# Optimization experiments

Measured on AMD Instinct MI355X. Metric: run time of the kernel, lower is better.

## Reference

```python
import jax, jax.numpy as jnp
import numpy as np

L, D, H, FF = 6, 1024, 16, 4096
HD = D // H
EPS = 1e-5


def _ln(x, g, b):
    m = jnp.mean(x, axis=-1, keepdims=True)
    v = jnp.var(x, axis=-1, keepdims=True)
    return (x - m) * jax.lax.rsqrt(v + EPS) * g + b


def _heads(t, S, B):  # [S,B,D] -> [B*H,S,HD]
    return t.reshape(S, B * H, HD).swapaxes(0, 1)


def _attn(q, k, v, mask):
    # q,k,v: [B*H, Sq/Sk, HD]; q pre-scaled
    scores = jnp.einsum('bqd,bkd->bqk', q, k)
    if mask is not None:
        scores = scores + mask  # broadcast [1,Sq,Sk]
    p = jax.nn.softmax(scores, axis=-1)
    return jnp.einsum('bqk,bkd->bqd', p, v)


def _self_attn(x, w_qkv, b_qkv, w_out, b_out, mask):
    S, B, _ = x.shape
    qkv = x @ w_qkv.T + b_qkv  # [S,B,3D]
    q, k, v = jnp.split(qkv, 3, axis=-1)
    q = q * (HD ** -0.5)
    a = _attn(_heads(q, S, B), _heads(k, S, B), _heads(v, S, B), mask)
    a = a.swapaxes(0, 1).reshape(S, B, D)
    return a @ w_out.T + b_out


def _cross_attn(x, mem, w_q, b_q, w_kv, b_kv, w_out, b_out):
    S, B, _ = x.shape
    Sm = mem.shape[0]
    q = (x @ w_q.T + b_q) * (HD ** -0.5)
    kv = mem @ w_kv.T + b_kv  # [Sm,B,2D]
    k, v = jnp.split(kv, 2, axis=-1)
    a = _attn(_heads(q, S, B), _heads(k, Sm, B), _heads(v, Sm, B), None)
    a = a.swapaxes(0, 1).reshape(S, B, D)
    return a @ w_out.T + b_out


def _ffn(x, w1, b1, w2, b2):
    h = jax.nn.gelu(x @ w1.T + b1, approximate=False)
    return h @ w2.T + b2


def setup_inputs() -> dict:
    key = jax.random.key(0)
    ks = iter(jax.random.split(key, 64))
    def p(*shape, s=0.02):
        return (jax.random.normal(next(ks), shape, dtype=jnp.float32) * s)
    inp = {
        'src': jax.random.normal(next(ks), (512, 8, D), dtype=jnp.float32),
        'tgt': jax.random.normal(next(ks), (512, 8, D), dtype=jnp.float32),
        # encoder params (stacked over L layers)
        'enc_qkv_w': p(L, 3 * D, D), 'enc_qkv_b': p(L, 3 * D),
        'enc_out_w': p(L, D, D), 'enc_out_b': p(L, D),
        'enc_ln1_g': jnp.ones((L, D)), 'enc_ln1_b': jnp.zeros((L, D)),
        'enc_fc1_w': p(L, FF, D), 'enc_fc1_b': p(L, FF),
        'enc_fc2_w': p(L, D, FF), 'enc_fc2_b': p(L, D),
        'enc_ln2_g': jnp.ones((L, D)), 'enc_ln2_b': jnp.zeros((L, D)),
        'enc_norm_g': jnp.ones((D,)), 'enc_norm_b': jnp.zeros((D,)),
        # decoder params
        'dec_qkv_w': p(L, 3 * D, D), 'dec_qkv_b': p(L, 3 * D),
        'dec_sout_w': p(L, D, D), 'dec_sout_b': p(L, D),
        'dec_ln1_g': jnp.ones((L, D)), 'dec_ln1_b': jnp.zeros((L, D)),
        'dec_q_w': p(L, D, D), 'dec_q_b': p(L, D),
        'dec_kv_w': p(L, 2 * D, D), 'dec_kv_b': p(L, 2 * D),
        'dec_cout_w': p(L, D, D), 'dec_cout_b': p(L, D),
        'dec_ln2_g': jnp.ones((L, D)), 'dec_ln2_b': jnp.zeros((L, D)),
        'dec_fc1_w': p(L, FF, D), 'dec_fc1_b': p(L, FF),
        'dec_fc2_w': p(L, D, FF), 'dec_fc2_b': p(L, D),
        'dec_ln3_g': jnp.ones((L, D)), 'dec_ln3_b': jnp.zeros((L, D)),
        'dec_norm_g': jnp.ones((D,)), 'dec_norm_b': jnp.zeros((D,)),
    }
    return inp


def reference(src, tgt,
              enc_qkv_w, enc_qkv_b, enc_out_w, enc_out_b,
              enc_ln1_g, enc_ln1_b, enc_fc1_w, enc_fc1_b,
              enc_fc2_w, enc_fc2_b, enc_ln2_g, enc_ln2_b,
              enc_norm_g, enc_norm_b,
              dec_qkv_w, dec_qkv_b, dec_sout_w, dec_sout_b,
              dec_ln1_g, dec_ln1_b, dec_q_w, dec_q_b,
              dec_kv_w, dec_kv_b, dec_cout_w, dec_cout_b,
              dec_ln2_g, dec_ln2_b, dec_fc1_w, dec_fc1_b,
              dec_fc2_w, dec_fc2_b, dec_ln3_g, dec_ln3_b,
              dec_norm_g, dec_norm_b):
    St = tgt.shape[0]
    # causal additive mask [1,St,St]
    causal = jnp.where(jnp.tril(jnp.ones((St, St), dtype=bool)), 0.0, -jnp.inf)
    causal = causal[None].astype(src.dtype)

    # ---- encoder ----
    x = src
    for i in range(L):
        x = x + _self_attn(_ln(x, enc_ln1_g[i], enc_ln1_b[i]),
                           enc_qkv_w[i], enc_qkv_b[i], enc_out_w[i], enc_out_b[i], None)
        x = x + _ffn(_ln(x, enc_ln2_g[i], enc_ln2_b[i]),
                     enc_fc1_w[i], enc_fc1_b[i], enc_fc2_w[i], enc_fc2_b[i])
    memory = _ln(x, enc_norm_g, enc_norm_b)

    # ---- decoder ----
    y = tgt
    for i in range(L):
        y = y + _self_attn(_ln(y, dec_ln1_g[i], dec_ln1_b[i]),
                           dec_qkv_w[i], dec_qkv_b[i], dec_sout_w[i], dec_sout_b[i], causal)
        y = y + _cross_attn(_ln(y, dec_ln2_g[i], dec_ln2_b[i]), memory,
                            dec_q_w[i], dec_q_b[i], dec_kv_w[i], dec_kv_b[i],
                            dec_cout_w[i], dec_cout_b[i])
        y = y + _ffn(_ln(y, dec_ln3_g[i], dec_ln3_b[i]),
                     dec_fc1_w[i], dec_fc1_b[i], dec_fc2_w[i], dec_fc2_b[i])
    return _ln(y, dec_norm_g, dec_norm_b)
```

## Files before the change

### kernel.cpp

```cpp
#include <hip/hip_runtime.h>

typedef __attribute__((ext_vector_type(4))) float f32x4;
typedef __attribute__((ext_vector_type(8))) short short8;
typedef unsigned int u32;
typedef unsigned short u16;
typedef __attribute__((ext_vector_type(2))) u32 u32x2;
typedef __attribute__((ext_vector_type(4))) u32 u32x4;

#define DEV __device__ __forceinline__
#define SB0  __builtin_amdgcn_sched_barrier(0)
#define HBAR asm volatile("s_barrier" ::: "memory")

DEV u16 f2b(float f){
  u32 u = __builtin_bit_cast(u32, f);
  u32 r = u + 0x7fffu + ((u >> 16) & 1u);
  return (u16)(r >> 16);
}
DEV u32 pk2(float a, float b){ return (u32)f2b(a) | ((u32)f2b(b) << 16); }

DEV void gload16(const void* g, void* l){
  __builtin_amdgcn_global_load_lds((const __attribute__((address_space(1))) void*)g,
                                   (__attribute__((address_space(3))) void*)l, 16, 0, 0);
}
DEV u32 lds_addr(void* p){
  return (u32)(unsigned long long)(__attribute__((address_space(3))) char*)p;
}

__global__ __launch_bounds__(256) void cvt_k(const float* __restrict__ in,
                                             u16* __restrict__ out, int n8)
{
  int i = blockIdx.x*256 + threadIdx.x;
  const int stride = gridDim.x*256;
  for (; i < n8; i += stride){
    const float4 a = ((const float4*)in)[2*i];
    const float4 b = ((const float4*)in)[2*i+1];
    u32x4 r;
    r.x = pk2(a.x,a.y); r.y = pk2(a.z,a.w);
    r.z = pk2(b.x,b.y); r.w = pk2(b.z,b.w);
    ((u32x4*)out)[i] = r;
  }
}

template<int OUT_F32>
__global__ __launch_bounds__(256) void ln_k(const float* __restrict__ x,
    const float* __restrict__ gam, const float* __restrict__ bet,
    void* __restrict__ out)
{
  const int row = blockIdx.x, tid = threadIdx.x;
  const float4 v = ((const float4*)(x + row*1024))[tid];
  float s = (v.x + v.y) + (v.z + v.w);
  float q = (v.x*v.x + v.y*v.y) + (v.z*v.z + v.w*v.w);
  #pragma unroll
  for (int m = 1; m < 64; m <<= 1){ s += __shfl_xor(s, m); q += __shfl_xor(q, m); }
  __shared__ float ps[4], pq[4];
  if ((tid & 63) == 0){ ps[tid>>6] = s; pq[tid>>6] = q; }
  __syncthreads();
  s = (ps[0]+ps[1]) + (ps[2]+ps[3]);
  q = (pq[0]+pq[1]) + (pq[2]+pq[3]);
  const float mean = s * (1.f/1024.f);
  const float var  = q * (1.f/1024.f) - mean*mean;
  const float rstd = rsqrtf(var + 1e-5f);
  const float4 gg = ((const float4*)gam)[tid];
  const float4 bb = ((const float4*)bet)[tid];
  const float o0 = (v.x-mean)*rstd*gg.x + bb.x;
  const float o1 = (v.y-mean)*rstd*gg.y + bb.y;
  const float o2 = (v.z-mean)*rstd*gg.z + bb.z;
  const float o3 = (v.w-mean)*rstd*gg.w + bb.w;
  if (OUT_F32){
    float4 r; r.x=o0; r.y=o1; r.z=o2; r.w=o3;
    ((float4*)out)[row*256 + tid] = r;
  } else {
    u32x2 r; r.x = pk2(o0,o1); r.y = pk2(o2,o3);
    ((u32x2*)out)[row*256 + tid] = r;
  }
}

__global__ __launch_bounds__(256) void reduce4_k(const float* __restrict__ p,
    const float* __restrict__ res, const float* __restrict__ bias,
    float* __restrict__ out)
{
  const int row = blockIdx.x, tid = threadIdx.x;
  const size_t MN = 4096ull*1024ull;
  const float4 b  = ((const float4*)bias)[tid];
  const float4 a0 = ((const float4*)(p + 0*MN + (size_t)row*1024))[tid];
  const float4 a1 = ((const float4*)(p + 1*MN + (size_t)row*1024))[tid];
  const float4 a2 = ((const float4*)(p + 2*MN + (size_t)row*1024))[tid];
  const float4 a3 = ((const float4*)(p + 3*MN + (size_t)row*1024))[tid];
  const float4 r  = ((const float4*)(res + (size_t)row*1024))[tid];
  float4 o;
  o.x = (a0.x+a1.x)+(a2.x+a3.x) + r.x + b.x;
  o.y = (a0.y+a1.y)+(a2.y+a3.y) + r.y + b.y;
  o.z = (a0.z+a1.z)+(a2.z+a3.z) + r.z + b.z;
  o.w = (a0.w+a1.w)+(a2.w+a3.w) + r.w + b.w;
  ((float4*)(out + (size_t)row*1024))[tid] = o;
}

template<int DO_GELU>
__global__ __launch_bounds__(512,2) void gemm256_k(
    const u16* __restrict__ A, const u16* __restrict__ W,
    const float* __restrict__ bias, u16* __restrict__ Cout,
    int M, int N, int K)
{
  __shared__ char lds[131072];
  const int tid = threadIdx.x;
  const int lane = tid & 63, wid = tid >> 6;
  const int wr = wid >> 2, wc = wid & 3;
  const int g = lane >> 4, c16 = lane & 15;

  const u32 nwg = gridDim.x * gridDim.y;
  u32 flat = blockIdx.x + gridDim.x * blockIdx.y;
  {
    const u32 q = nwg >> 3, r = nwg & 7;
    const u32 xcd = flat & 7, idx = flat >> 3;
    flat = (xcd < r ? xcd*(q+1) : r*(q+1) + (xcd-r)*q) + idx;
  }
  const int m0 = (int)(flat % gridDim.x) * 256;
  const int n0 = (int)(flat / gridDim.x) * 256;

  f32x4 acc[8][4];
  #pragma unroll
  for (int m = 0; m < 8; m++)
    #pragma unroll
    for (int n = 0; n < 4; n++) acc[m][n] = (f32x4){0.f,0.f,0.f,0.f};

  const int srow = tid >> 3, schk = tid & 7;
  const int scg = schk ^ (srow & 7);
  const u16* aS = A + (size_t)(m0 + srow)*K + scg*8;
  const u16* wS = W + (size_t)(n0 + srow)*K + scg*8;

  auto SG = [&](const u16* base, int regionOff, int sb, int half, int i, int kk){
    gload16(base + (size_t)(half*128 + i*64)*K + kk,
            lds + sb*65536 + regionOff + half*16384 + i*8192 + tid*16);
  };
  short8 af[4][2], bf[4][2];
  auto LDA4 = [&](char* bufA, int mbase){
    #pragma unroll
    for (int i = 0; i < 4; i++){
      const int r = (mbase + i)*16 + c16;
      const int rx = r & 7;
      af[i][0] = *(const short8*)(bufA + r*128 + ((g ^ rx) << 4));
      af[i][1] = *(const short8*)(bufA + r*128 + (((4 + g) ^ rx) << 4));
    }
  };
  auto LDB2 = [&](char* bufB, int nbase){
    #pragma unroll
    for (int i = 0; i < 2; i++){
      const int r = (wc & 1)*64 + (nbase + i)*16 + c16;
      const int rx = r & 7;
      bf[nbase+i][0] = *(const short8*)(bufB + r*128 + ((g ^ rx) << 4));
      bf[nbase+i][1] = *(const short8*)(bufB + r*128 + (((4 + g) ^ rx) << 4));
    }
  };

  const int NT = K >> 6;
  SG(wS, 32768, 0, 0, 0, 0); SG(wS, 32768, 0, 0, 1, 0);
  SG(wS, 32768, 0, 1, 0, 0); SG(wS, 32768, 0, 1, 1, 0);
  SG(aS, 0,     0, 0, 0, 0); SG(aS, 0,     0, 0, 1, 0);
  SG(aS, 0,     0, 1, 0, 0); SG(aS, 0,     0, 1, 1, 0);
  asm volatile("s_waitcnt vmcnt(1)" ::: "memory");
  HBAR;

  for (int t = 0; t < NT; ++t){
    const int b = t & 1, sb = b ^ 1;
    const int skk = (t+1) << 6;
    const bool st = (t+1 < NT);
    char* bufA = lds + b*65536 + wr*16384;
    char* bufB = lds + b*65536 + 32768 + (wc >> 1)*16384;

    LDA4(bufA, 0); LDB2(bufB, 0);
    if (st){ SG(wS, 32768, sb, 0, 0, skk); SG(wS, 32768, sb, 0, 1, skk); }
    HBAR;
    asm volatile("s_waitcnt lgkmcnt(0)" ::: "memory"); SB0;
    __builtin_amdgcn_s_setprio(1);
    #pragma unroll
    for (int ks = 0; ks < 2; ks++)
      #pragma unroll
      for (int i = 0; i < 4; i++)
        #pragma unroll
        for (int j = 0; j < 2; j++)
          acc[i][j] = __builtin_amdgcn_mfma_f32_16x16x32_bf16(af[i][ks], bf[j][ks], acc[i][j], 0,0,0);
    __builtin_amdgcn_s_setprio(0);
    LDB2(bufB, 2);
    if (st){ SG(wS, 32768, sb, 1, 0, skk); SG(wS, 32768, sb, 1, 1, skk); }
    HBAR;
    asm volatile("s_waitcnt lgkmcnt(0)" ::: "memory"); SB0;
    __builtin_amdgcn_s_setprio(1);
    #pragma unroll
    for (int ks = 0; ks < 2; ks++)
      #pragma unroll
      for (int i = 0; i < 4; i++)
        #pragma unroll
        for (int j = 2; j < 4; j++)
          acc[i][j] = __builtin_amdgcn_mfma_f32_16x16x32_bf16(af[i][ks], bf[j][ks], acc[i][j], 0,0,0);
    __builtin_amdgcn_s_setprio(0);
    if (st) asm volatile("s_waitcnt vmcnt(4)" ::: "memory");
    else    asm volatile("s_waitcnt vmcnt(0)" ::: "memory");
    HBAR;
    LDA4(bufA, 4);
    if (st){ SG(aS, 0, sb, 0, 0, skk); SG(aS, 0, sb, 0, 1, skk); }
    asm volatile("s_waitcnt lgkmcnt(0)" ::: "memory"); SB0;
    __builtin_amdgcn_s_setprio(1);
    #pragma unroll
    for (int ks = 0; ks < 2; ks++)
      #pragma unroll
      for (int i = 0; i < 4; i++)
        #pragma unroll
        for (int j = 0; j < 2; j++)
          acc[4+i][j] = __builtin_amdgcn_mfma_f32_16x16x32_bf16(af[i][ks], bf[j][ks], acc[4+i][j], 0,0,0);
    __builtin_amdgcn_s_setprio(0);
    if (st){ SG(aS, 0, sb, 1, 0, skk); SG(aS, 0, sb, 1, 1, skk); }
    HBAR;
    __builtin_amdgcn_s_setprio(1);
    #pragma unroll
    for (int ks = 0; ks < 2; ks++)
      #pragma unroll
      for (int i = 0; i < 4; i++)
        #pragma unroll
        for (int j = 2; j < 4; j++)
          acc[4+i][j] = __builtin_amdgcn_mfma_f32_16x16x32_bf16(af[i][ks], bf[j][ks], acc[4+i][j], 0,0,0);
    __builtin_amdgcn_s_setprio(0);
    if (st) asm volatile("s_waitcnt vmcnt(1)" ::: "memory");
    HBAR;
  }

  #pragma unroll
  for (int n = 0; n < 4; n++){
    const int col = n0 + wc*64 + n*16 + c16;
    const float bv = bias[col];
    #pragma unroll
    for (int m = 0; m < 8; m++){
      const int rbase = m0 + wr*128 + m*16 + g*4;
      #pragma unroll
      for (int r = 0; r < 4; r++){
        float v = acc[m][n][r] + bv;
        if (DO_GELU) v = 0.5f*v*(1.f + erff(v*0.70710678118654752f));
        Cout[(size_t)(rbase + r)*N + col] = f2b(v);
      }
    }
  }
}

template<int DO_GELU, int DO_RES, int OUT_F32>
__global__ __launch_bounds__(512,2) void gemm128p_k(
    const u16* __restrict__ A, const u16* __restrict__ W,
    const float* __restrict__ bias, const float* __restrict__ res,
    void* __restrict__ Cout, int M, int N, int K)
{
  __shared__ char lds[65536];
  const int tid = threadIdx.x;
  const int lane = tid & 63, wid = tid >> 6;
  const int wr = wid >> 2, wc = wid & 3;
  const int g = lane >> 4, c16 = lane & 15;

  const u32 nwg = gridDim.x * gridDim.y;
  u32 flat = blockIdx.x + gridDim.x * blockIdx.y;
  {
    const u32 q = nwg >> 3, r = nwg & 7;
    const u32 xcd = flat & 7, idx = flat >> 3;
    flat = (xcd < r ? xcd*(q+1) : r*(q+1) + (xcd-r)*q) + idx;
  }
  const int n0 = (int)(flat % gridDim.x) * 128;
  const int m0 = (int)(flat / gridDim.x) * 128;

  f32x4 acc[4][2];
  #pragma unroll
  for (int m = 0; m < 4; m++)
    #pragma unroll
    for (int n = 0; n < 2; n++) acc[m][n] = (f32x4){0.f,0.f,0.f,0.f};

  const int srow = tid >> 3, schk = tid & 7;
  const int scg = schk ^ (srow & 7);
  const u16* aS = A + (size_t)(m0 + srow)*K + scg*8;
  const u16* wS = W + (size_t)(n0 + srow)*K + scg*8;

  auto SG = [&](const u16* base, int regionOff, int sb, int i, int kk){
    gload16(base + (size_t)(i*64)*K + kk,
            lds + sb*32768 + regionOff + i*8192 + tid*16);
  };
  short8 af[2][2], af2[2][2], bf[2][2];
  auto LDA = [&](short8 (*dst)[2], char* bufA, int mbase){
    #pragma unroll
    for (int i = 0; i < 2; i++){
      const int r = wr*64 + (mbase + i)*16 + c16;
      const int rx = r & 7;
      dst[i][0] = *(const short8*)(bufA + r*128 + ((g ^ rx) << 4));
      dst[i][1] = *(const short8*)(bufA + r*128 + (((4 + g) ^ rx) << 4));
    }
  };
  auto LDB = [&](char* bufB){
    #pragma unroll
    for (int i = 0; i < 2; i++){
      const int r = wc*32 + i*16 + c16;
      const int rx = r & 7;
      bf[i][0] = *(const short8*)(bufB + r*128 + ((g ^ rx) << 4));
      bf[i][1] = *(const short8*)(bufB + r*128 + (((4 + g) ^ rx) << 4));
    }
  };

  const int NT = K >> 6;
  SG(wS, 16384, 0, 0, 0); SG(wS, 16384, 0, 1, 0);
  SG(aS, 0,     0, 0, 0); SG(aS, 0,     0, 1, 0);

  for (int t = 0; t < NT; ++t){
    const int b = t & 1, sb = b ^ 1;
    const int skk = (t+1) << 6;
    const bool st = (t+1 < NT);
    char* bufA = lds + b*32768;
    char* bufB = lds + b*32768 + 16384;

    if (st){ SG(wS, 16384, sb, 0, skk); SG(wS, 16384, sb, 1, skk); }
    if (st) asm volatile("s_waitcnt vmcnt(2)" ::: "memory");
    else    asm volatile("s_waitcnt vmcnt(0)" ::: "memory");
    HBAR;
    LDA(af, bufA, 0); LDB(bufB);
    if (st){ SG(aS, 0, sb, 0, skk); SG(aS, 0, sb, 1, skk); }
    asm volatile("s_waitcnt lgkmcnt(0)" ::: "memory"); SB0;
    __builtin_amdgcn_s_setprio(1);
    #pragma unroll
    for (int ks = 0; ks < 2; ks++)
      #pragma unroll
      for (int i = 0; i < 2; i++)
        #pragma unroll
        for (int j = 0; j < 2; j++)
          acc[i][j] = __builtin_amdgcn_mfma_f32_16x16x32_bf16(af[i][ks], bf[j][ks], acc[i][j], 0,0,0);
    __builtin_amdgcn_s_setprio(0);
    LDA(af2, bufA, 2);
    asm volatile("s_waitcnt lgkmcnt(0)" ::: "memory"); SB0;
    __builtin_amdgcn_s_setprio(1);
    #pragma unroll
    for (int ks = 0; ks < 2; ks++)
      #pragma unroll
      for (int i = 0; i < 2; i++)
        #pragma unroll
        for (int j = 0; j < 2; j++)
          acc[2+i][j] = __builtin_amdgcn_mfma_f32_16x16x32_bf16(af2[i][ks], bf[j][ks], acc[2+i][j], 0,0,0);
    __builtin_amdgcn_s_setprio(0);
    HBAR;
  }

  #pragma unroll
  for (int n = 0; n < 2; n++){
    const int col = n0 + wc*32 + n*16 + c16;
    const float bv = bias[col];
    #pragma unroll
    for (int m = 0; m < 4; m++){
      const int rbase = m0 + wr*64 + m*16 + g*4;
      #pragma unroll
      for (int r = 0; r < 4; r++){
        float v = acc[m][n][r] + bv;
        if (DO_GELU) v = 0.5f*v*(1.f + erff(v*0.70710678118654752f));
        if (DO_RES)  v += res[(size_t)(rbase + r)*N + col];
        if (OUT_F32) ((float*)Cout)[(size_t)(rbase + r)*N + col] = v;
        else         ((u16*)Cout)[(size_t)(rbase + r)*N + col] = f2b(v);
      }
    }
  }
}

__global__ __launch_bounds__(512,2) void gemmsk_k(
    const u16* __restrict__ A, const u16* __restrict__ W,
    float* __restrict__ part, int M, int N, int Kfull)
{
  __shared__ char lds[65536];
  const int tid = threadIdx.x;
  const int lane = tid & 63, wid = tid >> 6;
  const int wr = wid >> 2, wc = wid & 3;
  const int g = lane >> 4, c16 = lane & 15;
  const int k0 = (int)blockIdx.z << 10;

  const u32 nwg = gridDim.x * gridDim.y;
  u32 flat = blockIdx.x + gridDim.x * blockIdx.y;
  {
    const u32 q = nwg >> 3, r = nwg & 7;
    const u32 xcd = flat & 7, idx = flat >> 3;
    flat = (xcd < r ? xcd*(q+1) : r*(q+1) + (xcd-r)*q) + idx;
  }
  const int n0 = (int)(flat % gridDim.x) * 128;
  const int m0 = (int)(flat / gridDim.x) * 128;

  f32x4 acc[4][2];
  #pragma unroll
  for (int m = 0; m < 4; m++)
    #pragma unroll
    for (int n = 0; n < 2; n++) acc[m][n] = (f32x4){0.f,0.f,0.f,0.f};

  const int srow = tid >> 3, schk = tid & 7;
  const int scg = schk ^ (srow & 7);
  const u16* aS = A + (size_t)(m0 + srow)*Kfull + k0 + scg*8;
  const u16* wS = W + (size_t)(n0 + srow)*Kfull + k0 + scg*8;

  auto SG = [&](const u16* base, int regionOff, int sb, int i, int kk){
    gload16(base + (size_t)(i*64)*Kfull + kk,
            lds + sb*32768 + regionOff + i*8192 + tid*16);
  };
  short8 af[2][2], af2[2][2], bf[2][2];
  auto LDA = [&](short8 (*dst)[2], char* bufA, int mbase){
    #pragma unroll
    for (int i = 0; i < 2; i++){
      const int r = wr*64 + (mbase + i)*16 + c16;
      const int rx = r & 7;
      dst[i][0] = *(const short8*)(bufA + r*128 + ((g ^ rx) << 4));
      dst[i][1] = *(const short8*)(bufA + r*128 + (((4 + g) ^ rx) << 4));
    }
  };
  auto LDB = [&](char* bufB){
    #pragma unroll
    for (int i = 0; i < 2; i++){
      const int r = wc*32 + i*16 + c16;
      const int rx = r & 7;
      bf[i][0] = *(const short8*)(bufB + r*128 + ((g ^ rx) << 4));
      bf[i][1] = *(const short8*)(bufB + r*128 + (((4 + g) ^ rx) << 4));
    }
  };

  const int NT = 16;
  SG(wS, 16384, 0, 0, 0); SG(wS, 16384, 0, 1, 0);
  SG(aS, 0,     0, 0, 0); SG(aS, 0,     0, 1, 0);

  for (int t = 0; t < NT; ++t){
    const int b = t & 1, sb = b ^ 1;
    const int skk = (t+1) << 6;
    const bool st = (t+1 < NT);
    char* bufA = lds + b*32768;
    char* bufB = lds + b*32768 + 16384;

    if (st){ SG(wS, 16384, sb, 0, skk); SG(wS, 16384, sb, 1, skk); }
    if (st) asm volatile("s_waitcnt vmcnt(2)" ::: "memory");
    else    asm volatile("s_waitcnt vmcnt(0)" ::: "memory");
    HBAR;
    LDA(af, bufA, 0); LDB(bufB);
    if (st){ SG(aS, 0, sb, 0, skk); SG(aS, 0, sb, 1, skk); }
    asm volatile("s_waitcnt lgkmcnt(0)" ::: "memory"); SB0;
    __builtin_amdgcn_s_setprio(1);
    #pragma unroll
    for (int ks = 0; ks < 2; ks++)
      #pragma unroll
      for (int i = 0; i < 2; i++)
        #pragma unroll
        for (int j = 0; j < 2; j++)
          acc[i][j] = __builtin_amdgcn_mfma_f32_16x16x32_bf16(af[i][ks], bf[j][ks], acc[i][j], 0,0,0);
    __builtin_amdgcn_s_setprio(0);
    LDA(af2, bufA, 2);
    asm volatile("s_waitcnt lgkmcnt(0)" ::: "memory"); SB0;
    __builtin_amdgcn_s_setprio(1);
    #pragma unroll
    for (int ks = 0; ks < 2; ks++)
      #pragma unroll
      for (int i = 0; i < 2; i++)
        #pragma unroll
        for (int j = 0; j < 2; j++)
          acc[2+i][j] = __builtin_amdgcn_mfma_f32_16x16x32_bf16(af2[i][ks], bf[j][ks], acc[2+i][j], 0,0,0);
    __builtin_amdgcn_s_setprio(0);
    HBAR;
  }

  float* out = part + (size_t)blockIdx.z * ((size_t)M * N);
  #pragma unroll
  for (int n = 0; n < 2; n++){
    const int col = n0 + wc*32 + n*16 + c16;
    #pragma unroll
    for (int m = 0; m < 4; m++){
      const int rbase = m0 + wr*64 + m*16 + g*4;
      #pragma unroll
      for (int r = 0; r < 4; r++)
        out[(size_t)(rbase + r)*N + col] = acc[m][n][r];
    }
  }
}

template<int CAUSAL>
__global__ __launch_bounds__(256,4) void attn_k(
    const u16* __restrict__ Qb, int qB, int qS,
    const u16* __restrict__ Kb, int kB, int kS,
    const u16* __restrict__ Vb, int vB, int vS,
    u16* __restrict__ Ob, int oB, int oS, float scale)
{
  __shared__ char smem[32768];
  const int tid = threadIdx.x;
  const int lane = tid & 63, w = tid >> 6;
  const int g = lane >> 4, c16 = lane & 15;
  const int qt = blockIdx.x, bh = blockIdx.y;
  const int b = bh >> 4, h = bh & 15;
  const u16* Q  = Qb + b*qB + h*64;
  const u16* Kp = Kb + b*kB + h*64;
  const u16* Vp = Vb + b*vB + h*64;
  u16*       Op = Ob + b*oB + h*64;

  const int qrow = qt*64 + w*16 + c16;
  const short8 bq0 = *(const short8*)(Q + qrow*qS + g*8);
  const short8 bq1 = *(const short8*)(Q + qrow*qS + 32 + g*8);

  f32x4 o[4];
  #pragma unroll
  for (int d = 0; d < 4; d++) o[d] = (f32x4){0.f,0.f,0.f,0.f};
  float mrun = -__builtin_inff(), lrun = 0.f;

  const int srow = tid >> 3, schk = tid & 7;
  const u16* kSrc = Kp + srow*kS + (schk ^ (srow & 7))*8;
  const u16* vSrc = Vp + srow*vS + schk*8;
  const u32 vtr0 = lds_addr(smem) + 16384 + (8*g + (c16 >> 2))*128 + (c16 & 3)*8;

  auto STAGE = [&](int p, int j0){
    char* kb = smem + p*8192 + w*1024;
    char* vb = smem + 16384 + p*8192 + w*1024;
    gload16(kSrc + (size_t)j0*kS, kb);
    gload16(kSrc + (size_t)(j0+32)*kS, kb + 4096);
    gload16(vSrc + (size_t)j0*vS, vb);
    gload16(vSrc + (size_t)(j0+32)*vS, vb + 4096);
  };
  auto COMPUTE = [&](int p, int j0){
    char* Ks = smem + p*8192;
    f32x4 st[4];
    #pragma unroll
    for (int t = 0; t < 4; t++){
      const int row = t*16 + c16;
      const int rx = row & 7;
      const short8 ka0 = *(const short8*)(Ks + row*128 + ((g ^ rx) << 4));
      const short8 ka1 = *(const short8*)(Ks + row*128 + (((4 + g) ^ rx) << 4));
      f32x4 z = (f32x4){0.f,0.f,0.f,0.f};
      z = __builtin_amdgcn_mfma_f32_16x16x32_bf16(ka0, bq0, z, 0,0,0);
      z = __builtin_amdgcn_mfma_f32_16x16x32_bf16(ka1, bq1, z, 0,0,0);
      st[t] = z;
    }
    float mloc = -__builtin_inff();
    #pragma unroll
    for (int t = 0; t < 4; t++)
      #pragma unroll
      for (int r = 0; r < 4; r++){
        float sv = st[t][r]*scale;
        if (CAUSAL){ if (j0 + t*16 + g*4 + r > qrow) sv = -__builtin_inff(); }
        st[t][r] = sv;
        mloc = fmaxf(mloc, sv);
      }
    mloc = fmaxf(mloc, __shfl_xor(mloc, 16));
    mloc = fmaxf(mloc, __shfl_xor(mloc, 32));
    const float mnew = fmaxf(mrun, mloc);
    const float corr = __expf(mrun - mnew);
    float psum = 0.f;
    u32 pk[4][2];
    #pragma unroll
    for (int t = 0; t < 4; t++){
      const float p0 = __expf(st[t][0]-mnew), p1 = __expf(st[t][1]-mnew);
      const float p2 = __expf(st[t][2]-mnew), p3 = __expf(st[t][3]-mnew);
      psum += (p0+p1) + (p2+p3);
      pk[t][0] = pk2(p0,p1); pk[t][1] = pk2(p2,p3);
    }
    psum += __shfl_xor(psum, 16);
    psum += __shfl_xor(psum, 32);
    lrun = lrun*corr + psum;
    mrun = mnew;
    #pragma unroll
    for (int d = 0; d < 4; d++){
      o[d][0]*=corr; o[d][1]*=corr; o[d][2]*=corr; o[d][3]*=corr;
    }
    const int sl0 = c16 | (((g << 1)     & 3) << 4);
    const int sl1 = c16 | ((((g << 1)+1) & 3) << 4);
    const bool hi = g >= 2;
    union { short8 s; u32 u[4]; } pb, pb2;
    {
      const u32 a00 = (u32)__shfl((int)pk[0][0], sl0), a01 = (u32)__shfl((int)pk[0][1], sl0);
      const u32 a02 = (u32)__shfl((int)pk[0][0], sl1), a03 = (u32)__shfl((int)pk[0][1], sl1);
      const u32 a10 = (u32)__shfl((int)pk[1][0], sl0), a11 = (u32)__shfl((int)pk[1][1], sl0);
      const u32 a12 = (u32)__shfl((int)pk[1][0], sl1), a13 = (u32)__shfl((int)pk[1][1], sl1);
      pb.u[0] = hi ? a10 : a00;
      pb.u[1] = hi ? a11 : a01;
      pb.u[2] = hi ? a12 : a02;
      pb.u[3] = hi ? a13 : a03;
    }
    {
      const u32 a00 = (u32)__shfl((int)pk[2][0], sl0), a01 = (u32)__shfl((int)pk[2][1], sl0);
      const u32 a02 = (u32)__shfl((int)pk[2][0], sl1), a03 = (u32)__shfl((int)pk[2][1], sl1);
      const u32 a10 = (u32)__shfl((int)pk[3][0], sl0), a11 = (u32)__shfl((int)pk[3][1], sl0);
      const u32 a12 = (u32)__shfl((int)pk[3][0], sl1), a13 = (u32)__shfl((int)pk[3][1], sl1);
      pb2.u[0] = hi ? a10 : a00;
      pb2.u[1] = hi ? a11 : a01;
      pb2.u[2] = hi ? a12 : a02;
      pb2.u[3] = hi ? a13 : a03;
    }

    const u32 vtr = vtr0 + p*8192;
    u32x2 t00,t01,t10,t11,t20,t21,t30,t31;
    asm volatile("ds_read_b64_tr_b16 %0, %1 offset:0"   : "=v"(t00) : "v"(vtr));
    asm volatile("ds_read_b64_tr_b16 %0, %1 offset:512" : "=v"(t01) : "v"(vtr));
    asm volatile("ds_read_b64_tr_b16 %0, %1 offset:32"  : "=v"(t10) : "v"(vtr));
    asm volatile("ds_read_b64_tr_b16 %0, %1 offset:544" : "=v"(t11) : "v"(vtr));
    asm volatile("ds_read_b64_tr_b16 %0, %1 offset:64"  : "=v"(t20) : "v"(vtr));
    asm volatile("ds_read_b64_tr_b16 %0, %1 offset:576" : "=v"(t21) : "v"(vtr));
    asm volatile("ds_read_b64_tr_b16 %0, %1 offset:96"  : "=v"(t30) : "v"(vtr));
    asm volatile("ds_read_b64_tr_b16 %0, %1 offset:608" : "=v"(t31) : "v"(vtr));
    asm volatile("s_waitcnt lgkmcnt(0)" ::: "memory");
    __builtin_amdgcn_sched_barrier(0);
    {
      union { short8 s; u32x2 d[2]; } v0u, v1u, v2u, v3u;
      v0u.d[0]=t00; v0u.d[1]=t01;
      v1u.d[0]=t10; v1u.d[1]=t11;
      v2u.d[0]=t20; v2u.d[1]=t21;
      v3u.d[0]=t30; v3u.d[1]=t31;
      o[0] = __builtin_amdgcn_mfma_f32_16x16x32_bf16(v0u.s, pb.s, o[0], 0,0,0);
      o[1] = __builtin_amdgcn_mfma_f32_16x16x32_bf16(v1u.s, pb.s, o[1], 0,0,0);
      o[2] = __builtin_amdgcn_mfma_f32_16x16x32_bf16(v2u.s, pb.s, o[2], 0,0,0);
      o[3] = __builtin_amdgcn_mfma_f32_16x16x32_bf16(v3u.s, pb.s, o[3], 0,0,0);
    }
    asm volatile("ds_read_b64_tr_b16 %0, %1 offset:4096" : "=v"(t00) : "v"(vtr));
    asm volatile("ds_read_b64_tr_b16 %0, %1 offset:4608" : "=v"(t01) : "v"(vtr));
    asm volatile("ds_read_b64_tr_b16 %0, %1 offset:4128" : "=v"(t10) : "v"(vtr));
    asm volatile("ds_read_b64_tr_b16 %0, %1 offset:4640" : "=v"(t11) : "v"(vtr));
    asm volatile("ds_read_b64_tr_b16 %0, %1 offset:4160" : "=v"(t20) : "v"(vtr));
    asm volatile("ds_read_b64_tr_b16 %0, %1 offset:4672" : "=v"(t21) : "v"(vtr));
    asm volatile("ds_read_b64_tr_b16 %0, %1 offset:4192" : "=v"(t30) : "v"(vtr));
    asm volatile("ds_read_b64_tr_b16 %0, %1 offset:4704" : "=v"(t31) : "v"(vtr));
    asm volatile("s_waitcnt lgkmcnt(0)" ::: "memory");
    __builtin_amdgcn_sched_barrier(0);
    {
      union { short8 s; u32x2 d[2]; } v0u, v1u, v2u, v3u;
      v0u.d[0]=t00; v0u.d[1]=t01;
      v1u.d[0]=t10; v1u.d[1]=t11;
      v2u.d[0]=t20; v2u.d[1]=t21;
      v3u.d[0]=t30; v3u.d[1]=t31;
      o[0] = __builtin_amdgcn_mfma_f32_16x16x32_bf16(v0u.s, pb2.s, o[0], 0,0,0);
      o[1] = __builtin_amdgcn_mfma_f32_16x16x32_bf16(v1u.s, pb2.s, o[1], 0,0,0);
      o[2] = __builtin_amdgcn_mfma_f32_16x16x32_bf16(v2u.s, pb2.s, o[2], 0,0,0);
      o[3] = __builtin_amdgcn_mfma_f32_16x16x32_bf16(v3u.s, pb2.s, o[3], 0,0,0);
    }
  };

  const int nCh = CAUSAL ? (qt + 1) : 8;
  STAGE(0, 0);
  for (int jc = 0; jc < nCh - 1; ++jc){
    STAGE((jc+1) & 1, (jc+1)*64);
    asm volatile("s_waitcnt vmcnt(4)" ::: "memory");
    HBAR; SB0;
    COMPUTE(jc & 1, jc*64);
    SB0; HBAR;
  }
  asm volatile("s_waitcnt vmcnt(0)" ::: "memory");
  HBAR; SB0;
  COMPUTE((nCh-1) & 1, (nCh-1)*64);
  SB0; HBAR;

  const float inv = 1.f / lrun;
  char* Olds = smem;
  #pragma unroll
  for (int dd = 0; dd < 4; dd++){
    u32x2 val;
    val.x = pk2(o[dd][0]*inv, o[dd][1]*inv);
    val.y = pk2(o[dd][2]*inv, o[dd][3]*inv);
    const int row = w*16 + c16;
    const int off = 32*dd + 8*g;
    const int chunk = off >> 4, rem = off & 15;
    *(u32x2*)(Olds + row*128 + ((chunk ^ (row & 7)) << 4) + rem) = val;
  }
  __syncthreads();
  const int orow = tid >> 2, oc = tid & 3;
  #pragma unroll
  for (int i = 0; i < 2; i++){
    const int ch = oc*2 + i;
    const u32x4 vv = *(const u32x4*)(Olds + orow*128 + ((ch ^ (orow & 7)) << 4));
    *(u32x4*)(Op + (qt*64 + orow)*oS + ch*8) = vv;
  }
}

static inline int cvt_grid(int n8){ int g = (n8 + 255) / 256; return g > 2048 ? 2048 : g; }

extern "C" void kernel_launch(void* const* d_in, const int* in_sizes, int n_in,
                              void* d_out, int out_size, void* d_ws, size_t ws_size,
                              hipStream_t stream)
{
  (void)in_sizes; (void)n_in; (void)out_size; (void)ws_size;
  const float* src      = (const float*)d_in[0];
  const float* tgt      = (const float*)d_in[1];
  const float* e_qkv_w  = (const float*)d_in[2];
  const float* e_qkv_b  = (const float*)d_in[3];
  const float* e_out_w  = (const float*)d_in[4];
  const float* e_out_b  = (const float*)d_in[5];
  const float* e_ln1_g  = (const float*)d_in[6];
  const float* e_ln1_b  = (const float*)d_in[7];
  const float* e_fc1_w  = (const float*)d_in[8];
  const float* e_fc1_b  = (const float*)d_in[9];
  const float* e_fc2_w  = (const float*)d_in[10];
  const float* e_fc2_b  = (const float*)d_in[11];
  const float* e_ln2_g  = (const float*)d_in[12];
  const float* e_ln2_b  = (const float*)d_in[13];
  const float* e_nrm_g  = (const float*)d_in[14];
  const float* e_nrm_b  = (const float*)d_in[15];
  const float* dc_qkv_w = (const float*)d_in[16];
  const float* dc_qkv_b = (const float*)d_in[17];
  const float* dc_sout_w= (const float*)d_in[18];
  const float* dc_sout_b= (const float*)d_in[19];
  const float* dc_ln1_g = (const float*)d_in[20];
  const float* dc_ln1_b = (const float*)d_in[21];
  const float* dc_q_w   = (const float*)d_in[22];
  const float* dc_q_b   = (const float*)d_in[23];
  const float* dc_kv_w  = (const float*)d_in[24];
  const float* dc_kv_b  = (const float*)d_in[25];
  const float* dc_cout_w= (const float*)d_in[26];
  const float* dc_cout_b= (const float*)d_in[27];
  const float* dc_ln2_g = (const float*)d_in[28];
  const float* dc_ln2_b = (const float*)d_in[29];
  const float* dc_fc1_w = (const float*)d_in[30];
  const float* dc_fc1_b = (const float*)d_in[31];
  const float* dc_fc2_w = (const float*)d_in[32];
  const float* dc_fc2_b = (const float*)d_in[33];
  const float* dc_ln3_g = (const float*)d_in[34];
  const float* dc_ln3_b = (const float*)d_in[35];
  const float* dc_nrm_g = (const float*)d_in[36];
  const float* dc_nrm_b = (const float*)d_in[37];

  char* ws = (char*)d_ws;
  u16*  ln_out = (u16*)(ws);
  u16*  attn_o = (u16*)(ws + (8u<<20));
  u16*  membuf = (u16*)(ws + (16u<<20));
  float* xres  = (float*)(ws + (24u<<20));
  u16*  region = (u16*)(ws + (40u<<20));
  u16*  qkv   = region;
  u16*  hbuf  = region;
  u16*  qbuf  = region;
  u16*  kvbuf = region + (4u<<20);
  float* fparts = (float*)(ws + (432ull<<20));

  const dim3 blk(256);
  const dim3 blk512(512);
  const int M = 4096;

  u16* wb = (u16*)(ws + (72u<<20));
  size_t woff = 0;
  auto CV = [&](const float* wsrc, size_t n)->u16* {
    u16* p = wb + woff; woff += n;
    cvt_k<<<cvt_grid((int)(n >> 3)), blk, 0, stream>>>(wsrc, p, (int)(n >> 3));
    return p;
  };
  u16* Weqkv = CV(e_qkv_w,  6ull*3072*1024);
  u16* Weout = CV(e_out_w,  6ull*1024*1024);
  u16* Wefc1 = CV(e_fc1_w,  6ull*4096*1024);
  u16* Wefc2 = CV(e_fc2_w,  6ull*4096*1024);
  u16* Wdqkv = CV(dc_qkv_w, 6ull*3072*1024);
  u16* Wdsout= CV(dc_sout_w,6ull*1024*1024);
  u16* Wdq   = CV(dc_q_w,   6ull*1024*1024);
  u16* Wdkv  = CV(dc_kv_w,  6ull*2048*1024);
  u16* Wdcout= CV(dc_cout_w,6ull*1024*1024);
  u16* Wdfc1 = CV(dc_fc1_w, 6ull*4096*1024);
  u16* Wdfc2 = CV(dc_fc2_w, 6ull*4096*1024);

  for (int i = 0; i < 6; i++){
    const float* xin = i ? xres : src;
    ln_k<0><<<4096, blk, 0, stream>>>(xin, e_ln1_g + i*1024, e_ln1_b + i*1024, ln_out);
    gemm256_k<0><<<dim3(16, 12), blk512, 0, stream>>>(ln_out,
        Weqkv + (size_t)i*3145728, e_qkv_b + i*3072, qkv, M, 3072, 1024);
    attn_k<0><<<dim3(8,128), blk, 0, stream>>>(qkv, 3072, 24576,
        qkv+1024, 3072, 24576, qkv+2048, 3072, 24576, attn_o, 1024, 8192, 0.125f);
    gemm128p_k<0,1,1><<<dim3(8, 32), blk512, 0, stream>>>(attn_o,
        Weout + (size_t)i*1048576, e_out_b + i*1024, xin, xres, M, 1024, 1024);
    ln_k<0><<<4096, blk, 0, stream>>>(xres, e_ln2_g + i*1024, e_ln2_b + i*1024, ln_out);
    gemm256_k<1><<<dim3(16, 16), blk512, 0, stream>>>(ln_out,
        Wefc1 + (size_t)i*4194304, e_fc1_b + i*4096, hbuf, M, 4096, 1024);
    gemmsk_k<<<dim3(8, 32, 4), blk512, 0, stream>>>(hbuf,
        Wefc2 + (size_t)i*4194304, fparts, M, 1024, 4096);
    reduce4_k<<<4096, blk, 0, stream>>>(fparts, xres, e_fc2_b + i*1024, xres);
  }
  ln_k<0><<<4096, blk, 0, stream>>>(xres, e_nrm_g, e_nrm_b, membuf);

  for (int i = 0; i < 6; i++){
    const float* yin = i ? xres : tgt;
    ln_k<0><<<4096, blk, 0, stream>>>(yin, dc_ln1_g + i*1024, dc_ln1_b + i*1024, ln_out);
    gemm256_k<0><<<dim3(16, 12), blk512, 0, stream>>>(ln_out,
        Wdqkv + (size_t)i*3145728, dc_qkv_b + i*3072, qkv, M, 3072, 1024);
    attn_k<1><<<dim3(8,128), blk, 0, stream>>>(qkv, 3072, 24576,
        qkv+1024, 3072, 24576, qkv+2048, 3072, 24576, attn_o, 1024, 8192, 0.125f);
    gemm128p_k<0,1,1><<<dim3(8, 32), blk512, 0, stream>>>(attn_o,
        Wdsout + (size_t)i*1048576, dc_sout_b + i*1024, yin, xres, M, 1024, 1024);
    ln_k<0><<<4096, blk, 0, stream>>>(xres, dc_ln2_g + i*1024, dc_ln2_b + i*1024, ln_out);
    gemm128p_k<0,0,0><<<dim3(8, 32), blk512, 0, stream>>>(ln_out,
        Wdq + (size_t)i*1048576, dc_q_b + i*1024, nullptr, qbuf, M, 1024, 1024);
    gemm128p_k<0,0,0><<<dim3(16, 32), blk512, 0, stream>>>(membuf,
        Wdkv + (size_t)i*2097152, dc_kv_b + i*2048, nullptr, kvbuf, M, 2048, 1024);
    attn_k<0><<<dim3(8,128), blk, 0, stream>>>(qbuf, 1024, 8192,
        kvbuf, 2048, 16384, kvbuf+1024, 2048, 16384, attn_o, 1024, 8192, 0.125f);
    gemm128p_k<0,1,1><<<dim3(8, 32), blk512, 0, stream>>>(attn_o,
        Wdcout + (size_t)i*1048576, dc_cout_b + i*1024, xres, xres, M, 1024, 1024);
    ln_k<0><<<4096, blk, 0, stream>>>(xres, dc_ln3_g + i*1024, dc_ln3_b + i*1024, ln_out);
    gemm256_k<1><<<dim3(16, 16), blk512, 0, stream>>>(ln_out,
        Wdfc1 + (size_t)i*4194304, dc_fc1_b + i*4096, hbuf, M, 4096, 1024);
    gemmsk_k<<<dim3(8, 32, 4), blk512, 0, stream>>>(hbuf,
        Wdfc2 + (size_t)i*4194304, fparts, M, 1024, 4096);
    reduce4_k<<<4096, blk, 0, stream>>>(fparts, xres, dc_fc2_b + i*1024, xres);
  }
  ln_k<1><<<4096, blk, 0, stream>>>(xres, dc_nrm_g, dc_nrm_b, d_out);
}
```

Before: 3.362 ms.

## Replace split-K FC2 with fused full-K GEMM and merge cross-attn projections

FC2 no longer uses the 4-way split-K GEMM with fp32 partials and a separate reduce kernel. It now calls the 128-tile GEMM over the full K with bias and residual fused into the epilogue. The decoder's cross-attention Q and KV projections are combined into one launch through a new dual-GEMM kernel that splits workgroups between the two problems. This removes the partial-sum memory traffic and extra launches, at the cost of fewer workgroups and longer serial K loops for FC2.

```diff
diff --git a/kernel.cpp b/kernel.cpp
--- a/kernel.cpp
+++ b/kernel.cpp
@@ -75,26 +75,6 @@
   }
 }
 
-__global__ __launch_bounds__(256) void reduce4_k(const float* __restrict__ p,
-    const float* __restrict__ res, const float* __restrict__ bias,
-    float* __restrict__ out)
-{
-  const int row = blockIdx.x, tid = threadIdx.x;
-  const size_t MN = 4096ull*1024ull;
-  const float4 b  = ((const float4*)bias)[tid];
-  const float4 a0 = ((const float4*)(p + 0*MN + (size_t)row*1024))[tid];
-  const float4 a1 = ((const float4*)(p + 1*MN + (size_t)row*1024))[tid];
-  const float4 a2 = ((const float4*)(p + 2*MN + (size_t)row*1024))[tid];
-  const float4 a3 = ((const float4*)(p + 3*MN + (size_t)row*1024))[tid];
-  const float4 r  = ((const float4*)(res + (size_t)row*1024))[tid];
-  float4 o;
-  o.x = (a0.x+a1.x)+(a2.x+a3.x) + r.x + b.x;
-  o.y = (a0.y+a1.y)+(a2.y+a3.y) + r.y + b.y;
-  o.z = (a0.z+a1.z)+(a2.z+a3.z) + r.z + b.z;
-  o.w = (a0.w+a1.w)+(a2.w+a3.w) + r.w + b.w;
-  ((float4*)(out + (size_t)row*1024))[tid] = o;
-}
-
 template<int DO_GELU>
 __global__ __launch_bounds__(512,2) void gemm256_k(
     const u16* __restrict__ A, const u16* __restrict__ W,
@@ -240,6 +220,105 @@
   }
 }
 
+DEV void g128_body(const u16* __restrict__ A, const u16* __restrict__ W,
+                   const float* __restrict__ bias, u16* __restrict__ Cout,
+                   int N, int K, int m0, int n0, char* lds)
+{
+  const int tid = threadIdx.x;
+  const int lane = tid & 63, wid = tid >> 6;
+  const int wr = wid >> 2, wc = wid & 3;
+  const int g = lane >> 4, c16 = lane & 15;
+
+  f32x4 acc[4][2];
+  #pragma unroll
+  for (int m = 0; m < 4; m++)
+    #pragma unroll
+    for (int n = 0; n < 2; n++) acc[m][n] = (f32x4){0.f,0.f,0.f,0.f};
+
+  const int srow = tid >> 3, schk = tid & 7;
+  const int scg = schk ^ (srow & 7);
+  const u16* aS = A + (size_t)(m0 + srow)*K + scg*8;
+  const u16* wS = W + (size_t)(n0 + srow)*K + scg*8;
+
+  auto SG = [&](const u16* base, int regionOff, int sb, int i, int kk){
+    gload16(base + (size_t)(i*64)*K + kk,
+            lds + sb*32768 + regionOff + i*8192 + tid*16);
+  };
+  short8 af[2][2], af2[2][2], bf[2][2];
+  auto LDA = [&](short8 (*dst)[2], char* bufA, int mbase){
+    #pragma unroll
+    for (int i = 0; i < 2; i++){
+      const int r = wr*64 + (mbase + i)*16 + c16;
+      const int rx = r & 7;
+      dst[i][0] = *(const short8*)(bufA + r*128 + ((g ^ rx) << 4));
+      dst[i][1] = *(const short8*)(bufA + r*128 + (((4 + g) ^ rx) << 4));
+    }
+  };
+  auto LDB = [&](char* bufB){
+    #pragma unroll
+    for (int i = 0; i < 2; i++){
+      const int r = wc*32 + i*16 + c16;
+      const int rx = r & 7;
+      bf[i][0] = *(const short8*)(bufB + r*128 + ((g ^ rx) << 4));
+      bf[i][1] = *(const short8*)(bufB + r*128 + (((4 + g) ^ rx) << 4));
+    }
+  };
+
+  const int NT = K >> 6;
+  SG(wS, 16384, 0, 0, 0); SG(wS, 16384, 0, 1, 0);
+  SG(aS, 0,     0, 0, 0); SG(aS, 0,     0, 1, 0);
+
+  for (int t = 0; t < NT; ++t){
+    const int b = t & 1, sb = b ^ 1;
+    const int skk = (t+1) << 6;
+    const bool st = (t+1 < NT);
+    char* bufA = lds + b*32768;
+    char* bufB = lds + b*32768 + 16384;
+
+    if (st){ SG(wS, 16384, sb, 0, skk); SG(wS, 16384, sb, 1, skk); }
+    if (st) asm volatile("s_waitcnt vmcnt(2)" ::: "memory");
+    else    asm volatile("s_waitcnt vmcnt(0)" ::: "memory");
+    HBAR;
+    LDA(af, bufA, 0); LDB(bufB);
+    if (st){ SG(aS, 0, sb, 0, skk); SG(aS, 0, sb, 1, skk); }
+    asm volatile("s_waitcnt lgkmcnt(0)" ::: "memory"); SB0;
+    __builtin_amdgcn_s_setprio(1);
+    #pragma unroll
+    for (int ks = 0; ks < 2; ks++)
+      #pragma unroll
+      for (int i = 0; i < 2; i++)
+        #pragma unroll
+        for (int j = 0; j < 2; j++)
+          acc[i][j] = __builtin_amdgcn_mfma_f32_16x16x32_bf16(af[i][ks], bf[j][ks], acc[i][j], 0,0,0);
+    __builtin_amdgcn_s_setprio(0);
+    LDA(af2, bufA, 2);
+    asm volatile("s_waitcnt lgkmcnt(0)" ::: "memory"); SB0;
+    __builtin_amdgcn_s_setprio(1);
+    #pragma unroll
+    for (int ks = 0; ks < 2; ks++)
+      #pragma unroll
+      for (int i = 0; i < 2; i++)
+        #pragma unroll
+        for (int j = 0; j < 2; j++)
+          acc[2+i][j] = __builtin_amdgcn_mfma_f32_16x16x32_bf16(af2[i][ks], bf[j][ks], acc[2+i][j], 0,0,0);
+    __builtin_amdgcn_s_setprio(0);
+    HBAR;
+  }
+
+  #pragma unroll
+  for (int n = 0; n < 2; n++){
+    const int col = n0 + wc*32 + n*16 + c16;
+    const float bv = bias[col];
+    #pragma unroll
+    for (int m = 0; m < 4; m++){
+      const int rbase = m0 + wr*64 + m*16 + g*4;
+      #pragma unroll
+      for (int r = 0; r < 4; r++)
+        Cout[(size_t)(rbase + r)*N + col] = f2b(acc[m][n][r] + bv);
+    }
+  }
+}
+
 template<int DO_GELU, int DO_RES, int OUT_F32>
 __global__ __launch_bounds__(512,2) void gemm128p_k(
     const u16* __restrict__ A, const u16* __restrict__ W,
@@ -357,114 +436,32 @@
   }
 }
 
-__global__ __launch_bounds__(512,2) void gemmsk_k(
-    const u16* __restrict__ A, const u16* __restrict__ W,
-    float* __restrict__ part, int M, int N, int Kfull)
+__global__ __launch_bounds__(512,2) void gemmdual_k(
+    const u16* __restrict__ A0, const u16* __restrict__ W0,
+    const float* __restrict__ b0, u16* __restrict__ C0, int N0, int xb0,
+    const u16* __restrict__ A1, const u16* __restrict__ W1,
+    const float* __restrict__ b1, u16* __restrict__ C1, int N1,
+    int K)
 {
   __shared__ char lds[65536];
-  const int tid = threadIdx.x;
-  const int lane = tid & 63, wid = tid >> 6;
-  const int wr = wid >> 2, wc = wid & 3;
-  const int g = lane >> 4, c16 = lane & 15;
-  const int k0 = (int)blockIdx.z << 10;
-
-  const u32 nwg = gridDim.x * gridDim.y;
-  u32 flat = blockIdx.x + gridDim.x * blockIdx.y;
+  const u32 nwg = gridDim.x;
+  u32 flat = blockIdx.x;
   {
     const u32 q = nwg >> 3, r = nwg & 7;
     const u32 xcd = flat & 7, idx = flat >> 3;
     flat = (xcd < r ? xcd*(q+1) : r*(q+1) + (xcd-r)*q) + idx;
   }
-  const int n0 = (int)(flat % gridDim.x) * 128;
-  const int m0 = (int)(flat / gridDim.x) * 128;
-
-  f32x4 acc[4][2];
-  #pragma unroll
-  for (int m = 0; m < 4; m++)
-    #pragma unroll
-    for (int n = 0; n < 2; n++) acc[m][n] = (f32x4){0.f,0.f,0.f,0.f};
-
-  const int srow = tid >> 3, schk = tid & 7;
-  const int scg = schk ^ (srow & 7);
-  const u16* aS = A + (size_t)(m0 + srow)*Kfull + k0 + scg*8;
-  const u16* wS = W + (size_t)(n0 + srow)*Kfull + k0 + scg*8;
-
-  auto SG = [&](const u16* base, int regionOff, int sb, int i, int kk){
-    gload16(base + (size_t)(i*64)*Kfull + kk,
-            lds + sb*32768 + regionOff + i*8192 + tid*16);
-  };
-  short8 af[2][2], af2[2][2], bf[2][2];
-  auto LDA = [&](short8 (*dst)[2], char* bufA, int mbase){
-    #pragma unroll
-    for (int i = 0; i < 2; i++){
-      const int r = wr*64 + (mbase + i)*16 + c16;
-      const int rx = r & 7;
-      dst[i][0] = *(const short8*)(bufA + r*128 + ((g ^ rx) << 4));
-      dst[i][1] = *(const short8*)(bufA + r*128 + (((4 + g) ^ rx) << 4));
-    }
-  };
-  auto LDB = [&](char* bufB){
-    #pragma unroll
-    for (int i = 0; i < 2; i++){
-      const int r = wc*32 + i*16 + c16;
-      const int rx = r & 7;
-      bf[i][0] = *(const short8*)(bufB + r*128 + ((g ^ rx) << 4));
-      bf[i][1] = *(const short8*)(bufB + r*128 + (((4 + g) ^ rx) << 4));
-    }
-  };
-
-  const int NT = 16;
-  SG(wS, 16384, 0, 0, 0); SG(wS, 16384, 0, 1, 0);
-  SG(aS, 0,     0, 0, 0); SG(aS, 0,     0, 1, 0);
-
-  for (int t = 0; t < NT; ++t){
-    const int b = t & 1, sb = b ^ 1;
-    const int skk = (t+1) << 6;
-    const bool st = (t+1 < NT);
-    char* bufA = lds + b*32768;
-    char* bufB = lds + b*32768 + 16384;
-
-    if (st){ SG(wS, 16384, sb, 0, skk); SG(wS, 16384, sb, 1, skk); }
-    if (st) asm volatile("s_waitcnt vmcnt(2)" ::: "memory");
-    else    asm volatile("s_waitcnt vmcnt(0)" ::: "memory");
-    HBAR;
-    LDA(af, bufA, 0); LDB(bufB);
-    if (st){ SG(aS, 0, sb, 0, skk); SG(aS, 0, sb, 1, skk); }
-    asm volatile("s_waitcnt lgkmcnt(0)" ::: "memory"); SB0;
-    __builtin_amdgcn_s_setprio(1);
-    #pragma unroll
-    for (int ks = 0; ks < 2; ks++)
-      #pragma unroll
-      for (int i = 0; i < 2; i++)
-        #pragma unroll
-        for (int j = 0; j < 2; j++)
-          acc[i][j] = __builtin_amdgcn_mfma_f32_16x16x32_bf16(af[i][ks], bf[j][ks], acc[i][j], 0,0,0);
-    __builtin_amdgcn_s_setprio(0);
-    LDA(af2, bufA, 2);
-    asm volatile("s_waitcnt lgkmcnt(0)" ::: "memory"); SB0;
-    __builtin_amdgcn_s_setprio(1);
-    #pragma unroll
-    for (int ks = 0; ks < 2; ks++)
-      #pragma unroll
-      for (int i = 0; i < 2; i++)
-        #pragma unroll
-        for (int j = 0; j < 2; j++)
-          acc[2+i][j] = __builtin_amdgcn_mfma_f32_16x16x32_bf16(af2[i][ks], bf[j][ks], acc[2+i][j], 0,0,0);
-    __builtin_amdgcn_s_setprio(0);
-    HBAR;
-  }
-
-  float* out = part + (size_t)blockIdx.z * ((size_t)M * N);
-  #pragma unroll
-  for (int n = 0; n < 2; n++){
-    const int col = n0 + wc*32 + n*16 + c16;
-    #pragma unroll
-    for (int m = 0; m < 4; m++){
-      const int rbase = m0 + wr*64 + m*16 + g*4;
-      #pragma unroll
-      for (int r = 0; r < 4; r++)
-        out[(size_t)(rbase + r)*N + col] = acc[m][n][r];
-    }
+  const int seg0 = xb0 * 32;
+  if ((int)flat < seg0){
+    const int n0 = ((int)flat % xb0) * 128;
+    const int m0 = ((int)flat / xb0) * 128;
+    g128_body(A0, W0, b0, C0, N0, K, m0, n0, lds);
+  } else {
+    const int f = (int)flat - seg0;
+    const int xb1 = N1 >> 7;
+    const int n0 = (f % xb1) * 128;
+    const int m0 = (f / xb1) * 128;
+    g128_body(A1, W1, b1, C1, N1, K, m0, n0, lds);
   }
 }
 
@@ -716,7 +713,6 @@
   u16*  hbuf  = region;
   u16*  qbuf  = region;
   u16*  kvbuf = region + (4u<<20);
-  float* fparts = (float*)(ws + (432ull<<20));
 
   const dim3 blk(256);
   const dim3 blk512(512);
@@ -753,9 +749,8 @@
     ln_k<0><<<4096, blk, 0, stream>>>(xres, e_ln2_g + i*1024, e_ln2_b + i*1024, ln_out);
     gemm256_k<1><<<dim3(16, 16), blk512, 0, stream>>>(ln_out,
         Wefc1 + (size_t)i*4194304, e_fc1_b + i*4096, hbuf, M, 4096, 1024);
-    gemmsk_k<<<dim3(8, 32, 4), blk512, 0, stream>>>(hbuf,
-        Wefc2 + (size_t)i*4194304, fparts, M, 1024, 4096);
-    reduce4_k<<<4096, blk, 0, stream>>>(fparts, xres, e_fc2_b + i*1024, xres);
+    gemm128p_k<0,1,1><<<dim3(8, 32), blk512, 0, stream>>>(hbuf,
+        Wefc2 + (size_t)i*4194304, e_fc2_b + i*1024, xres, xres, M, 1024, 4096);
   }
   ln_k<0><<<4096, blk, 0, stream>>>(xres, e_nrm_g, e_nrm_b, membuf);
 
@@ -769,10 +764,10 @@
     gemm128p_k<0,1,1><<<dim3(8, 32), blk512, 0, stream>>>(attn_o,
         Wdsout + (size_t)i*1048576, dc_sout_b + i*1024, yin, xres, M, 1024, 1024);
     ln_k<0><<<4096, blk, 0, stream>>>(xres, dc_ln2_g + i*1024, dc_ln2_b + i*1024, ln_out);
-    gemm128p_k<0,0,0><<<dim3(8, 32), blk512, 0, stream>>>(ln_out,
-        Wdq + (size_t)i*1048576, dc_q_b + i*1024, nullptr, qbuf, M, 1024, 1024);
-    gemm128p_k<0,0,0><<<dim3(16, 32), blk512, 0, stream>>>(membuf,
-        Wdkv + (size_t)i*2097152, dc_kv_b + i*2048, nullptr, kvbuf, M, 2048, 1024);
+    gemmdual_k<<<dim3(768), blk512, 0, stream>>>(
+        ln_out, Wdq + (size_t)i*1048576, dc_q_b + i*1024, qbuf, 1024, 8,
+        membuf, Wdkv + (size_t)i*2097152, dc_kv_b + i*2048, kvbuf, 2048,
+        1024);
     attn_k<0><<<dim3(8,128), blk, 0, stream>>>(qbuf, 1024, 8192,
         kvbuf, 2048, 16384, kvbuf+1024, 2048, 16384, attn_o, 1024, 8192, 0.125f);
     gemm128p_k<0,1,1><<<dim3(8, 32), blk512, 0, stream>>>(attn_o,
@@ -780,9 +775,8 @@
     ln_k<0><<<4096, blk, 0, stream>>>(xres, dc_ln3_g + i*1024, dc_ln3_b + i*1024, ln_out);
     gemm256_k<1><<<dim3(16, 16), blk512, 0, stream>>>(ln_out,
         Wdfc1 + (size_t)i*4194304, dc_fc1_b + i*4096, hbuf, M, 4096, 1024);
-    gemmsk_k<<<dim3(8, 32, 4), blk512, 0, stream>>>(hbuf,
-        Wdfc2 + (size_t)i*4194304, fparts, M, 1024, 4096);
-    reduce4_k<<<4096, blk, 0, stream>>>(fparts, xres, dc_fc2_b + i*1024, xres);
+    gemm128p_k<0,1,1><<<dim3(8, 32), blk512, 0, stream>>>(hbuf,
+        Wdfc2 + (size_t)i*4194304, e_fc2_b == dc_fc2_b ? e_fc2_b : dc_fc2_b + i*1024, xres, xres, M, 1024, 4096);
   }
   ln_k<1><<<4096, blk, 0, stream>>>(xres, dc_nrm_g, dc_nrm_b, d_out);
 }
```

Result: faster. 3.169 ms (-5.8%).
